# Kernel optimization log

Hardware: AMD Instinct MI355X
Metric: run time of the kernel (lower is better)

Reference implementation:

```python
import jax, jax.numpy as jnp
import numpy as np

NUM_HEADS = 16
NUM_KV_HEADS = 4
ROPE_THETA = 10000.0


def apply_rope(x, position_ids, theta):
    # x: [B, S, h, d]; position_ids: [B, S]
    d = x.shape[-1]
    freqs = 1.0 / theta ** (jnp.arange(0, d, 2, dtype=jnp.float32) / d)  # [d/2]
    angles = position_ids.astype(jnp.float32)[..., None] * freqs          # [B, S, d/2]
    cos = jnp.cos(angles)[:, :, None, :]                                  # [B, S, 1, d/2]
    sin = jnp.sin(angles)[:, :, None, :]
    xr = x.astype(jnp.float32).reshape(*x.shape[:-1], d // 2, 2)
    x0, x1 = xr[..., 0], xr[..., 1]
    o0 = x0 * cos - x1 * sin
    o1 = x0 * sin + x1 * cos
    out = jnp.stack((o0, o1), axis=-1).reshape(*x.shape)
    return out.astype(x.dtype)


def setup_inputs() -> dict:
    key = jax.random.key(0)
    k0, k1, k2, k3, k4 = jax.random.split(key, 5)
    B, S, H = 1, 2048, 2048
    Hkv = H // (NUM_HEADS // NUM_KV_HEADS)  # 512
    init_scale = 0.02 / np.sqrt(H)
    return {
        "hidden_states": jax.random.normal(k0, (B, S, H), jnp.float32),
        "attention_mask": jnp.ones((B, S), jnp.int32),
        "segment_ids": jnp.zeros((B, S), jnp.int32),
        "position_ids": jnp.broadcast_to(jnp.arange(S, dtype=jnp.int32)[None], (B, S)),
        "Wq": jax.random.normal(k1, (H, H), jnp.float32) * init_scale,
        "Wk": jax.random.normal(k2, (H, Hkv), jnp.float32) * init_scale,
        "Wv": jax.random.normal(k3, (H, Hkv), jnp.float32) * init_scale,
        "Wo": jax.random.normal(k4, (H, H), jnp.float32) * init_scale,
    }


def reference(hidden_states, attention_mask, segment_ids, position_ids, Wq, Wk, Wv, Wo):
    B, S, H = hidden_states.shape
    nh, nkv = NUM_HEADS, NUM_KV_HEADS
    g = nh // nkv
    hd = H // nh

    xq = (hidden_states @ Wq).reshape(B, S, nh, hd)
    xk = (hidden_states @ Wk).reshape(B, S, nkv, hd)
    xv = (hidden_states @ Wv).reshape(B, S, nkv, hd)
    # GQA repeat: 'b s (h d) -> b s (h g) d' == repeat each kv head g times contiguously
    xk = jnp.repeat(xk, g, axis=2)  # [B, S, nh, hd]
    xv = jnp.repeat(xv, g, axis=2)

    xq = apply_rope(xq, position_ids, ROPE_THETA)
    xk = apply_rope(xk, position_ids, ROPE_THETA)

    # masks: causal AND padding AND segment
    causal = jnp.tril(jnp.ones((S, S), dtype=bool))[None, None]            # [1,1,S,S]
    pad = (attention_mask > 0)[:, None, None, :]                            # [B,1,1,S]
    seg = (segment_ids[:, :, None] == segment_ids[:, None, :])[:, None]     # [B,1,S,S]
    mask = causal & pad & seg                                               # [B,1,S,S]

    scale = 1.0 / np.sqrt(hd)
    logits = jnp.einsum("bqhd,bkhd->bhqk", xq.astype(jnp.float32), xk.astype(jnp.float32)) * scale
    logits = jnp.where(mask, logits, jnp.finfo(jnp.float32).min)
    probs = jax.nn.softmax(logits, axis=-1).astype(xv.dtype)
    attn = jnp.einsum("bhqk,bkhd->bqhd", probs, xv)                         # [B,S,nh,hd]

    out = attn.reshape(B, S, H) @ Wo
    return out
```

## Files before the change

kernel.cpp:

```cpp
#include <hip/hip_runtime.h>
#include <hip/hip_bf16.h>
#include <stdint.h>
#include <math.h>

#define SS 2048
#define HH 2048
#define NH 16
#define NKV 4
#define HD 128
#define HKV 512
#define NQKV 3072

typedef __bf16 bf16x8 __attribute__((ext_vector_type(8)));
typedef float f32x4 __attribute__((ext_vector_type(4)));

static_assert(sizeof(bf16x8) == 16, "bf16x8 must be 16B");

__device__ __forceinline__ void async_ld16(const void* gp, void* lp) {
  __builtin_amdgcn_global_load_lds(
      (const __attribute__((address_space(1))) unsigned int*)(uintptr_t)gp,
      (__attribute__((address_space(3))) unsigned int*)(uintptr_t)lp,
      16, 0, 0);
}

__device__ __forceinline__ unsigned short f2bu(float f) {
  __hip_bfloat16 b = __float2bfloat16(f);
  return *reinterpret_cast<unsigned short*>(&b);
}

__global__ __launch_bounds__(256) void k_prep1(
    const float* __restrict__ X, const float* __restrict__ Wq, const float* __restrict__ Wk,
    const float* __restrict__ Wv, const float* __restrict__ Wo,
    const int* __restrict__ amv, const int* __restrict__ seg, int* __restrict__ kseg,
    float2* __restrict__ rtab,
    __hip_bfloat16* __restrict__ Xb, __hip_bfloat16* __restrict__ WqT,
    __hip_bfloat16* __restrict__ WkT, __hip_bfloat16* __restrict__ WvT,
    __hip_bfloat16* __restrict__ WoT) {
  __shared__ float tile[32][33];
  int b = blockIdx.x;
  if (b < 4096) {
    int i = b * 256 + threadIdx.y * 32 + threadIdx.x;
    float4 v = ((const float4*)X)[i];
    ushort4 o;
    o.x = f2bu(v.x); o.y = f2bu(v.y); o.z = f2bu(v.z); o.w = f2bu(v.w);
    ((ushort4*)Xb)[i] = o;
    return;
  }
  b -= 4096;
  if (b >= 10248) {
    int i = (b - 10248) * 256 + threadIdx.y * 32 + threadIdx.x;
    int p = i >> 6, f = i & 63;
    const float L2T_D64 = 0.20762050593046837f;
    float freq = exp2f(-L2T_D64 * (float)f);
    float sn, cs;
    sincosf((float)p * freq, &sn, &cs);
    rtab[i] = make_float2(sn, cs);
    return;
  }
  if (b >= 10240) {
    int i = (b - 10240) * 256 + threadIdx.y * 32 + threadIdx.x;
    kseg[i] = (amv[i] > 0) ? seg[i] : 0x7fffffff;
    return;
  }
  const float* src; __hip_bfloat16* dst; int xtiles;
  if (b < 4096)      { src = Wq; dst = WqT; xtiles = 64; }
  else if (b < 8192) { src = Wo; dst = WoT; xtiles = 64; b -= 4096; }
  else if (b < 9216) { src = Wk; dst = WkT; xtiles = 16; b -= 8192; }
  else               { src = Wv; dst = WvT; xtiles = 16; b -= 9216; }
  const int C = xtiles * 32;
  int bx = (b % xtiles) * 32;
  int by = (b / xtiles) * 32;
  int tx = threadIdx.x, ty = threadIdx.y;
#pragma unroll
  for (int i = 0; i < 4; i++)
    tile[ty + i * 8][tx] = src[(size_t)(by + ty + i * 8) * C + bx + tx];
  __syncthreads();
#pragma unroll
  for (int i = 0; i < 4; i++)
    dst[(size_t)(bx + ty + i * 8) * HH + by + tx] = __float2bfloat16(tile[tx][ty + i * 8]);
}

__global__ __launch_bounds__(256, 2) void k_gemm_qkv(
    const __hip_bfloat16* __restrict__ A, const __hip_bfloat16* __restrict__ B,
    __hip_bfloat16* __restrict__ Qb, __hip_bfloat16* __restrict__ Kb,
    __hip_bfloat16* __restrict__ Vt, const int* __restrict__ pos,
    const float2* __restrict__ rtab) {
  __shared__ __align__(16) __hip_bfloat16 sA0[64 * 64];
  __shared__ __align__(16) __hip_bfloat16 sA1[64 * 64];
  __shared__ __align__(16) __hip_bfloat16 sA2[64 * 64];
  __shared__ __align__(16) __hip_bfloat16 sB0[128 * 64];
  __shared__ __align__(16) __hip_bfloat16 sB1[128 * 64];
  __shared__ __align__(16) __hip_bfloat16 sB2[128 * 64];
  const int tid = threadIdx.x;
  const int lane = tid & 63;
  const int wave = tid >> 6;
  const int bm = blockIdx.y * 64;
  const int bn = blockIdx.x * 128;
  const int wm = (wave & 1) * 32;
  const int wn = (wave >> 1) * 64;
  const int am = lane & 15;
  const int ch = lane >> 4;

  f32x4 acc[2][4] = {};

  auto stage = [&](__hip_bfloat16* sA, __hip_bfloat16* sB, int k0) {
#pragma unroll
    for (int q = 0; q < 2; q++) {
      int c = q * 256 + tid;
      int row = c >> 3, kp = c & 7;
      int col = (kp ^ (row & 7)) * 8;
      async_ld16(A + (size_t)(bm + row) * HH + k0 + col, (char*)sA + c * 16);
    }
#pragma unroll
    for (int q = 0; q < 4; q++) {
      int c = q * 256 + tid;
      int row = c >> 3, kp = c & 7;
      int col = (kp ^ (row & 7)) * 8;
      async_ld16(B + (size_t)(bn + row) * HH + k0 + col, (char*)sB + c * 16);
    }
  };
  auto compute = [&](const __hip_bfloat16* sA, const __hip_bfloat16* sB) {
#pragma unroll
    for (int kb = 0; kb < 2; kb++) {
      bf16x8 a[2], b[4];
#pragma unroll
      for (int i = 0; i < 2; i++) {
        int row = wm + i * 16 + am;
        a[i] = *(const bf16x8*)(sA + row * 64 + (((kb * 4 + ch) ^ (row & 7)) * 8));
      }
#pragma unroll
      for (int j = 0; j < 4; j++) {
        int row = wn + j * 16 + am;
        b[j] = *(const bf16x8*)(sB + row * 64 + (((kb * 4 + ch) ^ (row & 7)) * 8));
      }
#pragma unroll
      for (int i = 0; i < 2; i++)
#pragma unroll
        for (int j = 0; j < 4; j++)
          acc[i][j] = __builtin_amdgcn_mfma_f32_16x16x32_bf16(a[i], b[j], acc[i][j], 0, 0, 0);
    }
  };

  __hip_bfloat16 *cA = sA0, *nA = sA1, *fA = sA2;
  __hip_bfloat16 *cB = sB0, *nB = sB1, *fB = sB2;
  stage(cA, cB, 0);
  stage(nA, nB, 64);
  for (int t = 0; t < 32; ++t) {
    if (t + 1 < 32) asm volatile("s_waitcnt vmcnt(6)" ::: "memory");
    else            asm volatile("s_waitcnt vmcnt(0)" ::: "memory");
    asm volatile("s_barrier" ::: "memory");
    if (t + 2 < 32) stage(fA, fB, (t + 2) * 64);
    compute(cA, cB);
    __hip_bfloat16* tp;
    tp = cA; cA = nA; nA = fA; fA = tp;
    tp = cB; cB = nB; nB = fB; fB = tp;
  }

  const bool isV = (bn >= HH + HKV);
  if (isV) {
#pragma unroll
    for (int j = 0; j < 4; j++) {
      int lc = bn + wn + j * 16 + am - (HH + HKV);
#pragma unroll
      for (int i = 0; i < 2; i++) {
        int row = bm + wm + i * 16 + ch * 4;
        ushort4 o;
        o.x = f2bu(acc[i][j][0]); o.y = f2bu(acc[i][j][1]);
        o.z = f2bu(acc[i][j][2]); o.w = f2bu(acc[i][j][3]);
        *(ushort4*)(Vt + (size_t)lc * SS + row) = o;
      }
    }
  } else {
    const float SCLQ = 0.08838834764831845f * 1.4426950408889634f;
    const bool isQ = (bn < HH);
    int pint[2][4];
#pragma unroll
    for (int i = 0; i < 2; i++)
#pragma unroll
      for (int r = 0; r < 4; r++)
        pint[i][r] = pos[bm + wm + i * 16 + ch * 4 + r];
    const float sgn = (am & 1) ? 1.0f : -1.0f;
#pragma unroll
    for (int j = 0; j < 4; j++) {
      int col = bn + wn + j * 16 + am;
      int lc = isQ ? col : (col - HH);
      int fidx = (lc >> 1) & 63;
#pragma unroll
      for (int i = 0; i < 2; i++)
#pragma unroll
        for (int r = 0; r < 4; r++) {
          float v = acc[i][j][r];
          float px = __shfl_xor(v, 1, 64);
          float2 sc = rtab[pint[i][r] * 64 + fidx];
          float o = v * sc.y + sgn * px * sc.x;
          int row = bm + wm + i * 16 + ch * 4 + r;
          if (isQ) Qb[(size_t)row * HH + col] = __float2bfloat16(o * SCLQ);
          else     Kb[(size_t)row * HKV + lc] = __float2bfloat16(o);
        }
    }
  }
}

__global__ __launch_bounds__(256, 2) void k_gemm_out(
    const __hip_bfloat16* __restrict__ A, const __hip_bfloat16* __restrict__ B,
    float* __restrict__ C) {
  __shared__ __align__(16) __hip_bfloat16 sA0[64 * 64];
  __shared__ __align__(16) __hip_bfloat16 sA1[64 * 64];
  __shared__ __align__(16) __hip_bfloat16 sA2[64 * 64];
  __shared__ __align__(16) __hip_bfloat16 sB0[128 * 64];
  __shared__ __align__(16) __hip_bfloat16 sB1[128 * 64];
  __shared__ __align__(16) __hip_bfloat16 sB2[128 * 64];
  const int tid = threadIdx.x;
  const int lane = tid & 63;
  const int wave = tid >> 6;
  const int bm = blockIdx.y * 64;
  const int bn = blockIdx.x * 128;
  const int wm = (wave & 1) * 32;
  const int wn = (wave >> 1) * 64;
  const int am = lane & 15;
  const int ch = lane >> 4;

  f32x4 acc[2][4] = {};

  auto stage = [&](__hip_bfloat16* sA, __hip_bfloat16* sB, int k0) {
#pragma unroll
    for (int q = 0; q < 2; q++) {
      int c = q * 256 + tid;
      int row = c >> 3, kp = c & 7;
      int col = (kp ^ (row & 7)) * 8;
      async_ld16(A + (size_t)(bm + row) * HH + k0 + col, (char*)sA + c * 16);
    }
#pragma unroll
    for (int q = 0; q < 4; q++) {
      int c = q * 256 + tid;
      int row = c >> 3, kp = c & 7;
      int col = (kp ^ (row & 7)) * 8;
      async_ld16(B + (size_t)(bn + row) * HH + k0 + col, (char*)sB + c * 16);
    }
  };
  auto compute = [&](const __hip_bfloat16* sA, const __hip_bfloat16* sB) {
#pragma unroll
    for (int kb = 0; kb < 2; kb++) {
      bf16x8 a[2], b[4];
#pragma unroll
      for (int i = 0; i < 2; i++) {
        int row = wm + i * 16 + am;
        a[i] = *(const bf16x8*)(sA + row * 64 + (((kb * 4 + ch) ^ (row & 7)) * 8));
      }
#pragma unroll
      for (int j = 0; j < 4; j++) {
        int row = wn + j * 16 + am;
        b[j] = *(const bf16x8*)(sB + row * 64 + (((kb * 4 + ch) ^ (row & 7)) * 8));
      }
#pragma unroll
      for (int i = 0; i < 2; i++)
#pragma unroll
        for (int j = 0; j < 4; j++)
          acc[i][j] = __builtin_amdgcn_mfma_f32_16x16x32_bf16(a[i], b[j], acc[i][j], 0, 0, 0);
    }
  };

  __hip_bfloat16 *cA = sA0, *nA = sA1, *fA = sA2;
  __hip_bfloat16 *cB = sB0, *nB = sB1, *fB = sB2;
  stage(cA, cB, 0);
  stage(nA, nB, 64);
  for (int t = 0; t < 32; ++t) {
    if (t + 1 < 32) asm volatile("s_waitcnt vmcnt(6)" ::: "memory");
    else            asm volatile("s_waitcnt vmcnt(0)" ::: "memory");
    asm volatile("s_barrier" ::: "memory");
    if (t + 2 < 32) stage(fA, fB, (t + 2) * 64);
    compute(cA, cB);
    __hip_bfloat16* tp;
    tp = cA; cA = nA; nA = fA; fA = tp;
    tp = cB; cB = nB; nB = fB; fB = tp;
  }

#pragma unroll
  for (int i = 0; i < 2; i++)
#pragma unroll
    for (int j = 0; j < 4; j++)
#pragma unroll
      for (int r = 0; r < 4; r++) {
        int row = bm + wm + i * 16 + ch * 4 + r;
        int col = bn + wn + j * 16 + am;
        C[(size_t)row * HH + col] = acc[i][j][r];
      }
}

__global__ __launch_bounds__(512, 4) void k_attn(
    const __hip_bfloat16* __restrict__ Qb,
    const __hip_bfloat16* __restrict__ Kb,
    const __hip_bfloat16* __restrict__ Vt,
    const int* __restrict__ seg,
    const int* __restrict__ kseg,
    float* __restrict__ Obuf,
    float* __restrict__ Lbuf) {
  __shared__ __align__(16) __hip_bfloat16 sK[2][64 * 128];
  __shared__ __align__(16) __hip_bfloat16 sV[2][128 * 64];
  __shared__ __align__(16) __hip_bfloat16 sPall[8][16 * 64];

  const int bid = blockIdx.x;
  const int g = bid >> 5;
  const int qt = (bid < 256) ? (15 - g) : (g - 8);
  const int h = (bid >> 1) & 15;
  const int half = bid & 1;
  const int n0 = qt + 1;
  const int kt0 = half ? n0 : 0;
  const int kt1 = half ? (2 * qt + 2) : n0;

  const int kvh = h >> 2;
  const int tid = threadIdx.x, lane = tid & 63, w = tid >> 6;
  const int am = lane & 15, ch = lane >> 4;
  const int qrow0 = qt * 128 + w * 16;
  char* sP = (char*)&sPall[w][0];

  bf16x8 qf[4];
#pragma unroll
  for (int ks = 0; ks < 4; ks++)
    qf[ks] = *(const bf16x8*)(Qb + (size_t)(qrow0 + am) * HH + h * HD + ks * 32 + ch * 8);

  int segq[4];
#pragma unroll
  for (int r = 0; r < 4; r++) segq[r] = seg[qrow0 + ch * 4 + r];
  const int q0 = seg[qt * 128 + w * 16];
  const bool quni = __all((segq[0] == q0) && (segq[1] == q0) &&
                          (segq[2] == q0) && (segq[3] == q0));

  f32x4 o_acc[8] = {};
  float l_s[4] = {0.f, 0.f, 0.f, 0.f};

  auto stage = [&](int kt, int p) {
#pragma unroll
    for (int q = 0; q < 2; q++) {
      int c = q * 512 + tid;
      int row = c >> 4, kp = c & 15;
      int col = (kp ^ (row & 15)) * 8;
      async_ld16(Kb + (size_t)(kt * 64 + row) * HKV + kvh * 128 + col, (char*)sK[p] + c * 16);
    }
#pragma unroll
    for (int q = 0; q < 2; q++) {
      int c = q * 512 + tid;
      int row = c >> 3, kp = c & 7;
      int col = (kp ^ (row & 7)) * 8;
      async_ld16(Vt + (size_t)(kvh * 128 + row) * SS + kt * 64 + col, (char*)sV[p] + c * 16);
    }
  };

  stage(kt0, 0);
  for (int kt = kt0; kt < kt1; kt++) {
    const int p = (kt - kt0) & 1;
    const int kbase = kt * 64;
    const bool skip = (kbase > qrow0 + 15);
    __syncthreads();

    int kinfo[4];
    if (!skip) {
#pragma unroll
      for (int jt = 0; jt < 4; jt++) kinfo[jt] = kseg[kbase + jt * 16 + am];
    }
    if (kt + 1 < kt1) stage(kt + 1, p ^ 1);
    if (!skip) {
      f32x4 sacc[4] = {};
      __builtin_amdgcn_s_setprio(1);
#pragma unroll
      for (int ks = 0; ks < 4; ks++)
#pragma unroll
        for (int jt = 0; jt < 4; jt++) {
          bf16x8 kf = *(const bf16x8*)(sK[p] + (jt * 16 + am) * 128 + (((ks * 4 + ch) ^ am) * 8));
          sacc[jt] = __builtin_amdgcn_mfma_f32_16x16x32_bf16(qf[ks], kf, sacc[jt], 0, 0, 0);
        }
      __builtin_amdgcn_s_setprio(0);

      const bool needc = (kbase + 63 > qrow0);
      const bool fast = quni && !needc &&
          __all((kinfo[0] == q0) && (kinfo[1] == q0) &&
                (kinfo[2] == q0) && (kinfo[3] == q0));

      if (fast) {
#pragma unroll
        for (int jt = 0; jt < 4; jt++)
#pragma unroll
          for (int r = 0; r < 4; r++) {
            float pv = exp2f(sacc[jt][r] - 8.0f);
            l_s[r] += pv;
            int row = ch * 4 + r;
            int chunk = (jt * 2 + (am >> 3)) ^ (row & 7);
            *(__hip_bfloat16*)(sP + row * 128 + chunk * 16 + (am & 7) * 2) =
                __float2bfloat16(pv);
          }
      } else {
#pragma unroll
        for (int jt = 0; jt < 4; jt++) {
          int kk = kbase + jt * 16 + am;
#pragma unroll
          for (int r = 0; r < 4; r++) {
            int qrow = qrow0 + ch * 4 + r;
            bool ok = (kinfo[jt] == segq[r]) && (kk <= qrow);
            float pv = ok ? exp2f(sacc[jt][r] - 8.0f) : 0.0f;
            l_s[r] += pv;
            int row = ch * 4 + r;
            int chunk = (jt * 2 + (am >> 3)) ^ (row & 7);
            *(__hip_bfloat16*)(sP + row * 128 + chunk * 16 + (am & 7) * 2) =
                __float2bfloat16(pv);
          }
        }
      }

      __builtin_amdgcn_s_setprio(1);
#pragma unroll
      for (int ks = 0; ks < 2; ks++) {
        bf16x8 pf = *(const bf16x8*)(sP + am * 128 + (((ks * 4 + ch) ^ (am & 7)) * 16));
#pragma unroll
        for (int jt = 0; jt < 8; jt++) {
          int vrow = jt * 16 + am;
          bf16x8 vf = *(const bf16x8*)(sV[p] + vrow * 64 + (((ks * 4 + ch) ^ (vrow & 7)) * 8));
          o_acc[jt] = __builtin_amdgcn_mfma_f32_16x16x32_bf16(pf, vf, o_acc[jt], 0, 0, 0);
        }
      }
      __builtin_amdgcn_s_setprio(0);
    }
  }

#pragma unroll
  for (int off = 1; off < 16; off <<= 1)
#pragma unroll
    for (int r = 0; r < 4; r++) l_s[r] += __shfl_xor(l_s[r], off, 64);
  if (am == 0)
#pragma unroll
    for (int r = 0; r < 4; r++)
      unsafeAtomicAdd(Lbuf + (size_t)(qrow0 + ch * 4 + r) * NH + h, l_s[r]);
#pragma unroll
  for (int jt = 0; jt < 8; jt++)
#pragma unroll
    for (int r = 0; r < 4; r++) {
      int row = qrow0 + ch * 4 + r;
      unsafeAtomicAdd(Obuf + (size_t)row * HH + h * HD + jt * 16 + am, o_acc[jt][r]);
    }
}

__global__ __launch_bounds__(256) void k_norm(
    const float* __restrict__ Obuf, const float* __restrict__ Lbuf,
    __hip_bfloat16* __restrict__ Ab) {
  int i = blockIdx.x * 256 + threadIdx.x;
  int s = i >> 9;
  int hIdx = (i & 511) >> 5;
  float inv = 1.0f / Lbuf[(size_t)s * NH + hIdx];
  float4 v = ((const float4*)Obuf)[i];
  ushort4 o;
  o.x = f2bu(v.x * inv); o.y = f2bu(v.y * inv);
  o.z = f2bu(v.z * inv); o.w = f2bu(v.w * inv);
  ((ushort4*)Ab)[i] = o;
}

extern "C" void kernel_launch(void* const* d_in, const int* in_sizes, int n_in,
                              void* d_out, int out_size, void* d_ws, size_t ws_size,
                              hipStream_t stream) {
  const float* X  = (const float*)d_in[0];
  const int* amv  = (const int*)d_in[1];
  const int* seg  = (const int*)d_in[2];
  const int* pos  = (const int*)d_in[3];
  const float* Wq = (const float*)d_in[4];
  const float* Wk = (const float*)d_in[5];
  const float* Wv = (const float*)d_in[6];
  const float* Wo = (const float*)d_in[7];
  float* out = (float*)d_out;

  char* ws = (char*)d_ws;
  size_t off = 0;
  auto alloc = [&](size_t bytes) { void* p = ws + off; off += (bytes + 255) & ~(size_t)255; return p; };
  __hip_bfloat16* Xb   = (__hip_bfloat16*)alloc((size_t)SS * HH * 2);
  __hip_bfloat16* WqT  = (__hip_bfloat16*)alloc((size_t)HH * HH * 2);
  __hip_bfloat16* WkT  = (__hip_bfloat16*)alloc((size_t)HKV * HH * 2);
  __hip_bfloat16* WvT  = (__hip_bfloat16*)alloc((size_t)HKV * HH * 2);
  __hip_bfloat16* WoT  = (__hip_bfloat16*)alloc((size_t)HH * HH * 2);
  __hip_bfloat16* Qb   = (__hip_bfloat16*)alloc((size_t)SS * HH * 2);
  __hip_bfloat16* Kb   = (__hip_bfloat16*)alloc((size_t)SS * HKV * 2);
  __hip_bfloat16* Vt   = (__hip_bfloat16*)alloc((size_t)HKV * SS * 2);
  __hip_bfloat16* Ab   = (__hip_bfloat16*)alloc((size_t)SS * HH * 2);
  float*          Obuf = (float*)alloc((size_t)SS * HH * 4);
  float*          Lbuf = (float*)alloc((size_t)SS * NH * 4);
  int*            kseg = (int*)alloc((size_t)SS * 4);
  float2*         rtab = (float2*)alloc((size_t)SS * 64 * 8);
  (void)WkT; (void)WvT;

  hipMemsetAsync(Obuf, 0, (size_t)SS * HH * 4 + ((size_t)SS * NH * 4 + 255 & ~(size_t)255), stream);
  k_prep1<<<dim3(14856), dim3(32, 8), 0, stream>>>(X, Wq, Wk, Wv, Wo, amv, seg, kseg, rtab,
                                                   Xb, WqT, WkT, WvT, WoT);
  k_gemm_qkv<<<dim3(NQKV / 128, SS / 64), 256, 0, stream>>>(Xb, WqT, Qb, Kb, Vt, pos, rtab);
  k_attn<<<dim3(512), dim3(512), 0, stream>>>(Qb, Kb, Vt, seg, kseg, Obuf, Lbuf);
  k_norm<<<dim3(SS * HH / 4 / 256), 256, 0, stream>>>(Obuf, Lbuf, Ab);
  k_gemm_out<<<dim3(HH / 128, SS / 64), 256, 0, stream>>>(Ab, WoT, out);
}
```

Measured before the change: 246.4 us.

## Shrink attention q-tiles to 64 rows and double-buffer output GEMM

The attention kernel moves from 128-row query tiles with 8 waves to 64-row tiles with 4 waves, launched as 1024 blocks. Each head's KV range is split into two halves, and blocks with an empty range return early. This removes the per-wave causal skip branch and the old tile pairing, aiming for finer load balance and lower per-block resources. Separately, the output GEMM drops from triple to double LDS buffering with __syncthreads, so launch bounds can allow three blocks per CU, trading prefetch depth for occupancy.

```diff
diff --git a/kernel.cpp b/kernel.cpp
--- a/kernel.cpp
+++ b/kernel.cpp
@@ -201,15 +201,13 @@
   }
 }
 
-__global__ __launch_bounds__(256, 2) void k_gemm_out(
+__global__ __launch_bounds__(256, 3) void k_gemm_out(
     const __hip_bfloat16* __restrict__ A, const __hip_bfloat16* __restrict__ B,
     float* __restrict__ C) {
   __shared__ __align__(16) __hip_bfloat16 sA0[64 * 64];
+  __shared__ __align__(16) __hip_bfloat16 sB0[128 * 64];
   __shared__ __align__(16) __hip_bfloat16 sA1[64 * 64];
-  __shared__ __align__(16) __hip_bfloat16 sA2[64 * 64];
-  __shared__ __align__(16) __hip_bfloat16 sB0[128 * 64];
   __shared__ __align__(16) __hip_bfloat16 sB1[128 * 64];
-  __shared__ __align__(16) __hip_bfloat16 sB2[128 * 64];
   const int tid = threadIdx.x;
   const int lane = tid & 63;
   const int wave = tid >> 6;
@@ -260,19 +258,17 @@
     }
   };
 
-  __hip_bfloat16 *cA = sA0, *nA = sA1, *fA = sA2;
-  __hip_bfloat16 *cB = sB0, *nB = sB1, *fB = sB2;
-  stage(cA, cB, 0);
-  stage(nA, nB, 64);
-  for (int t = 0; t < 32; ++t) {
-    if (t + 1 < 32) asm volatile("s_waitcnt vmcnt(6)" ::: "memory");
-    else            asm volatile("s_waitcnt vmcnt(0)" ::: "memory");
-    asm volatile("s_barrier" ::: "memory");
-    if (t + 2 < 32) stage(fA, fB, (t + 2) * 64);
-    compute(cA, cB);
-    __hip_bfloat16* tp;
-    tp = cA; cA = nA; nA = fA; fA = tp;
-    tp = cB; cB = nB; nB = fB; fB = tp;
+  stage(sA0, sB0, 0);
+  int k0 = 0;
+  while (true) {
+    __syncthreads();
+    if (k0 + 64 < HH) stage(sA1, sB1, k0 + 64);
+    compute(sA0, sB0);
+    k0 += 64; if (k0 >= HH) break;
+    __syncthreads();
+    if (k0 + 64 < HH) stage(sA0, sB0, k0 + 64);
+    compute(sA1, sB1);
+    k0 += 64; if (k0 >= HH) break;
   }
 
 #pragma unroll
@@ -287,7 +283,7 @@
       }
 }
 
-__global__ __launch_bounds__(512, 4) void k_attn(
+__global__ __launch_bounds__(256, 2) void k_attn(
     const __hip_bfloat16* __restrict__ Qb,
     const __hip_bfloat16* __restrict__ Kb,
     const __hip_bfloat16* __restrict__ Vt,
@@ -297,21 +293,22 @@
     float* __restrict__ Lbuf) {
   __shared__ __align__(16) __hip_bfloat16 sK[2][64 * 128];
   __shared__ __align__(16) __hip_bfloat16 sV[2][128 * 64];
-  __shared__ __align__(16) __hip_bfloat16 sPall[8][16 * 64];
+  __shared__ __align__(16) __hip_bfloat16 sPall[4][16 * 64];
 
   const int bid = blockIdx.x;
-  const int g = bid >> 5;
-  const int qt = (bid < 256) ? (15 - g) : (g - 8);
+  const int qt = 31 - (bid >> 5);
   const int h = (bid >> 1) & 15;
   const int half = bid & 1;
-  const int n0 = qt + 1;
+  const int T = qt + 1;
+  const int n0 = (T + 1) >> 1;
   const int kt0 = half ? n0 : 0;
-  const int kt1 = half ? (2 * qt + 2) : n0;
+  const int kt1 = half ? T : n0;
+  if (kt0 >= kt1) return;
 
   const int kvh = h >> 2;
   const int tid = threadIdx.x, lane = tid & 63, w = tid >> 6;
   const int am = lane & 15, ch = lane >> 4;
-  const int qrow0 = qt * 128 + w * 16;
+  const int qrow0 = qt * 64 + w * 16;
   char* sP = (char*)&sPall[w][0];
 
   bf16x8 qf[4];
@@ -322,7 +319,7 @@
   int segq[4];
 #pragma unroll
   for (int r = 0; r < 4; r++) segq[r] = seg[qrow0 + ch * 4 + r];
-  const int q0 = seg[qt * 128 + w * 16];
+  const int q0 = seg[qrow0];
   const bool quni = __all((segq[0] == q0) && (segq[1] == q0) &&
                           (segq[2] == q0) && (segq[3] == q0));
 
@@ -331,15 +328,15 @@
 
   auto stage = [&](int kt, int p) {
 #pragma unroll
-    for (int q = 0; q < 2; q++) {
-      int c = q * 512 + tid;
+    for (int q = 0; q < 4; q++) {
+      int c = q * 256 + tid;
       int row = c >> 4, kp = c & 15;
       int col = (kp ^ (row & 15)) * 8;
       async_ld16(Kb + (size_t)(kt * 64 + row) * HKV + kvh * 128 + col, (char*)sK[p] + c * 16);
     }
 #pragma unroll
-    for (int q = 0; q < 2; q++) {
-      int c = q * 512 + tid;
+    for (int q = 0; q < 4; q++) {
+      int c = q * 256 + tid;
       int row = c >> 3, kp = c & 7;
       int col = (kp ^ (row & 7)) * 8;
       async_ld16(Vt + (size_t)(kvh * 128 + row) * SS + kt * 64 + col, (char*)sV[p] + c * 16);
@@ -350,75 +347,72 @@
   for (int kt = kt0; kt < kt1; kt++) {
     const int p = (kt - kt0) & 1;
     const int kbase = kt * 64;
-    const bool skip = (kbase > qrow0 + 15);
     __syncthreads();
 
     int kinfo[4];
-    if (!skip) {
-#pragma unroll
-      for (int jt = 0; jt < 4; jt++) kinfo[jt] = kseg[kbase + jt * 16 + am];
-    }
+#pragma unroll
+    for (int jt = 0; jt < 4; jt++) kinfo[jt] = kseg[kbase + jt * 16 + am];
+
     if (kt + 1 < kt1) stage(kt + 1, p ^ 1);
-    if (!skip) {
-      f32x4 sacc[4] = {};
-      __builtin_amdgcn_s_setprio(1);
-#pragma unroll
-      for (int ks = 0; ks < 4; ks++)
-#pragma unroll
-        for (int jt = 0; jt < 4; jt++) {
-          bf16x8 kf = *(const bf16x8*)(sK[p] + (jt * 16 + am) * 128 + (((ks * 4 + ch) ^ am) * 8));
-          sacc[jt] = __builtin_amdgcn_mfma_f32_16x16x32_bf16(qf[ks], kf, sacc[jt], 0, 0, 0);
+
+    f32x4 sacc[4] = {};
+    __builtin_amdgcn_s_setprio(1);
+#pragma unroll
+    for (int ks = 0; ks < 4; ks++)
+#pragma unroll
+      for (int jt = 0; jt < 4; jt++) {
+        bf16x8 kf = *(const bf16x8*)(sK[p] + (jt * 16 + am) * 128 + (((ks * 4 + ch) ^ am) * 8));
+        sacc[jt] = __builtin_amdgcn_mfma_f32_16x16x32_bf16(qf[ks], kf, sacc[jt], 0, 0, 0);
+      }
+    __builtin_amdgcn_s_setprio(0);
+
+    const bool needc = (kbase + 63 > qrow0);
+    const bool fast = quni && !needc &&
+        __all((kinfo[0] == q0) && (kinfo[1] == q0) &&
+              (kinfo[2] == q0) && (kinfo[3] == q0));
+
+    if (fast) {
+#pragma unroll
+      for (int jt = 0; jt < 4; jt++)
+#pragma unroll
+        for (int r = 0; r < 4; r++) {
+          float pv = exp2f(sacc[jt][r] - 8.0f);
+          l_s[r] += pv;
+          int row = ch * 4 + r;
+          int chunk = (jt * 2 + (am >> 3)) ^ (row & 7);
+          *(__hip_bfloat16*)(sP + row * 128 + chunk * 16 + (am & 7) * 2) =
+              __float2bfloat16(pv);
         }
-      __builtin_amdgcn_s_setprio(0);
-
-      const bool needc = (kbase + 63 > qrow0);
-      const bool fast = quni && !needc &&
-          __all((kinfo[0] == q0) && (kinfo[1] == q0) &&
-                (kinfo[2] == q0) && (kinfo[3] == q0));
-
-      if (fast) {
-#pragma unroll
-        for (int jt = 0; jt < 4; jt++)
-#pragma unroll
-          for (int r = 0; r < 4; r++) {
-            float pv = exp2f(sacc[jt][r] - 8.0f);
-            l_s[r] += pv;
-            int row = ch * 4 + r;
-            int chunk = (jt * 2 + (am >> 3)) ^ (row & 7);
-            *(__hip_bfloat16*)(sP + row * 128 + chunk * 16 + (am & 7) * 2) =
-                __float2bfloat16(pv);
-          }
-      } else {
-#pragma unroll
-        for (int jt = 0; jt < 4; jt++) {
-          int kk = kbase + jt * 16 + am;
-#pragma unroll
-          for (int r = 0; r < 4; r++) {
-            int qrow = qrow0 + ch * 4 + r;
-            bool ok = (kinfo[jt] == segq[r]) && (kk <= qrow);
-            float pv = ok ? exp2f(sacc[jt][r] - 8.0f) : 0.0f;
-            l_s[r] += pv;
-            int row = ch * 4 + r;
-            int chunk = (jt * 2 + (am >> 3)) ^ (row & 7);
-            *(__hip_bfloat16*)(sP + row * 128 + chunk * 16 + (am & 7) * 2) =
-                __float2bfloat16(pv);
-          }
+    } else {
+#pragma unroll
+      for (int jt = 0; jt < 4; jt++) {
+        int kk = kbase + jt * 16 + am;
+#pragma unroll
+        for (int r = 0; r < 4; r++) {
+          int qrow = qrow0 + ch * 4 + r;
+          bool ok = (kinfo[jt] == segq[r]) && (kk <= qrow);
+          float pv = ok ? exp2f(sacc[jt][r] - 8.0f) : 0.0f;
+          l_s[r] += pv;
+          int row = ch * 4 + r;
+          int chunk = (jt * 2 + (am >> 3)) ^ (row & 7);
+          *(__hip_bfloat16*)(sP + row * 128 + chunk * 16 + (am & 7) * 2) =
+              __float2bfloat16(pv);
         }
       }
-
-      __builtin_amdgcn_s_setprio(1);
-#pragma unroll
-      for (int ks = 0; ks < 2; ks++) {
-        bf16x8 pf = *(const bf16x8*)(sP + am * 128 + (((ks * 4 + ch) ^ (am & 7)) * 16));
-#pragma unroll
-        for (int jt = 0; jt < 8; jt++) {
-          int vrow = jt * 16 + am;
-          bf16x8 vf = *(const bf16x8*)(sV[p] + vrow * 64 + (((ks * 4 + ch) ^ (vrow & 7)) * 8));
-          o_acc[jt] = __builtin_amdgcn_mfma_f32_16x16x32_bf16(pf, vf, o_acc[jt], 0, 0, 0);
-        }
-      }
-      __builtin_amdgcn_s_setprio(0);
-    }
+    }
+
+    __builtin_amdgcn_s_setprio(1);
+#pragma unroll
+    for (int ks = 0; ks < 2; ks++) {
+      bf16x8 pf = *(const bf16x8*)(sP + am * 128 + (((ks * 4 + ch) ^ (am & 7)) * 16));
+#pragma unroll
+      for (int jt = 0; jt < 8; jt++) {
+        int vrow = jt * 16 + am;
+        bf16x8 vf = *(const bf16x8*)(sV[p] + vrow * 64 + (((ks * 4 + ch) ^ (vrow & 7)) * 8));
+        o_acc[jt] = __builtin_amdgcn_mfma_f32_16x16x32_bf16(pf, vf, o_acc[jt], 0, 0, 0);
+      }
+    }
+    __builtin_amdgcn_s_setprio(0);
   }
 
 #pragma unroll
@@ -487,7 +481,7 @@
   k_prep1<<<dim3(14856), dim3(32, 8), 0, stream>>>(X, Wq, Wk, Wv, Wo, amv, seg, kseg, rtab,
                                                    Xb, WqT, WkT, WvT, WoT);
   k_gemm_qkv<<<dim3(NQKV / 128, SS / 64), 256, 0, stream>>>(Xb, WqT, Qb, Kb, Vt, pos, rtab);
-  k_attn<<<dim3(512), dim3(512), 0, stream>>>(Qb, Kb, Vt, seg, kseg, Obuf, Lbuf);
+  k_attn<<<dim3(1024), 256, 0, stream>>>(Qb, Kb, Vt, seg, kseg, Obuf, Lbuf);
   k_norm<<<dim3(SS * HH / 4 / 256), 256, 0, stream>>>(Obuf, Lbuf, Ab);
   k_gemm_out<<<dim3(HH / 128, SS / 64), 256, 0, stream>>>(Ab, WoT, out);
 }
```

Result: faster. 236.5 us (-4.0%).
